# Optimization experiments

Hardware: AMD Instinct MI355X
Metric: run time of the kernel (lower is better)

Reference implementation:

```python
import jax, jax.numpy as jnp
import numpy as np

BATCH = 8
TABLE_NUM = 16          # levels L
TABLE_DIM = 8192        # entries per table
RES_MIN, RES_MAX = 16, 256
SAMPLE_RES = 256
N = SAMPLE_RES * SAMPLE_RES
CH = TABLE_NUM * 2      # feature dim per level is 2
STYLE_DIM = 512
PRIME = np.uint32(2654435761)
LN_EPS = 1e-5
DEMOD_EPS = 1e-8

# geometric level resolutions (Instant-NGP style)
_b = np.exp((np.log(RES_MAX) - np.log(RES_MIN)) / (TABLE_NUM - 1))
RES_LIST = [int(np.floor(RES_MIN * (_b ** l))) for l in range(TABLE_NUM)]


def _corner_idx_weights(coords):
    """coords [N,2] in [0,1] -> (idx [L,N,4] int32 flat into L*T, w [L,N,4])."""
    idx_all, w_all = [], []
    for l, res in enumerate(RES_LIST):
        pos = coords * (res - 1)                     # [N,2]
        p0f = jnp.floor(pos)
        frac = pos - p0f                              # bilinear fractions
        p0 = jnp.clip(p0f.astype(jnp.int32), 0, res - 2)
        x0, y0 = p0[:, 0], p0[:, 1]
        x1, y1 = x0 + 1, y0 + 1
        fx, fy = frac[:, 0], frac[:, 1]
        cx = jnp.stack([x0, x1, x0, x1], -1)          # [N,4]
        cy = jnp.stack([y0, y0, y1, y1], -1)
        w = jnp.stack([(1 - fx) * (1 - fy), fx * (1 - fy),
                       (1 - fx) * fy, fx * fy], -1)   # [N,4]
        if res * res <= TABLE_DIM:                    # dense grid fits: direct index
            idx = cy * res + cx
        else:                                         # spatial hash
            h = cx.astype(jnp.uint32) ^ (cy.astype(jnp.uint32) * PRIME)
            idx = (h % jnp.uint32(TABLE_DIM)).astype(jnp.int32)
        idx_all.append(idx + l * TABLE_DIM)
        w_all.append(w)
    return jnp.stack(idx_all), jnp.stack(w_all)       # [L,N,4]


def _hash_retrieve(tables, idx, w):
    """tables [B,L,T,2] -> bilinear multi-res lookup [B,N,2L]."""
    B = tables.shape[0]
    tf = tables.reshape(B, TABLE_NUM * TABLE_DIM, 2)
    g = tf[:, idx.reshape(-1)]                        # [B, L*N*4, 2]
    g = g.reshape(B, TABLE_NUM, N, 4, 2)
    feats = jnp.einsum('blncf,lnc->blnf', g, w)       # [B,L,N,2]
    return feats.transpose(0, 2, 1, 3).reshape(B, N, CH)


def _hash_recon(tokens, idx, w):
    """tokens [B,N,2L] -> transpose scatter back into tables [B,L,T,2]."""
    B = tokens.shape[0]
    t = tokens.reshape(B, N, TABLE_NUM, 2).transpose(0, 2, 1, 3)   # [B,L,N,2]
    contrib = jnp.einsum('blnf,lnc->blncf', t, w)                   # [B,L,N,4,2]
    out = jnp.zeros((B, TABLE_NUM * TABLE_DIM, 2), tokens.dtype)
    out = out.at[:, idx.reshape(-1)].add(contrib.reshape(B, -1, 2))
    return out.reshape(B, TABLE_NUM, TABLE_DIM, 2)


def _synthesis_layer(x, s, affine_w, affine_b, conv_w, conv_b):
    """StyleGAN2 modulated 3x3 conv (demodulate, up=1) + bias + lrelu*sqrt(2)."""
    styles = s @ (affine_w.T / np.sqrt(STYLE_DIM)) + affine_b       # [B,ch]
    xm = x * styles[:, :, None, None]                               # modulate input
    y = jax.lax.conv_general_dilated(xm, conv_w, (1, 1), [(1, 1), (1, 1)],
                                     dimension_numbers=('NCHW', 'OIHW', 'NCHW'))
    # demod coef: rsqrt(sum_{i,k,l} (w_oikl * style_i)^2 + eps)
    dcoef = jax.lax.rsqrt(jnp.einsum('oikl,bi->bo', conv_w * conv_w,
                                     styles * styles) + DEMOD_EPS)
    y = y * dcoef[:, :, None, None] + conv_b[None, :, None, None]
    return jax.nn.leaky_relu(y, 0.2) * np.sqrt(2.0)


def setup_inputs() -> dict:
    key = jax.random.key(0)
    k1, k2, k3, k4 = jax.random.split(key, 4)
    inputs = jax.random.normal(k1, (BATCH, TABLE_NUM, 2 * TABLE_DIM), jnp.float32)
    s = jax.random.normal(k2, (BATCH, STYLE_DIM), jnp.float32)
    g = jnp.linspace(0.0, 1.0, SAMPLE_RES)
    yy, xx = jnp.meshgrid(g, g, indexing='ij')
    coords = jnp.stack([xx, yy], -1).reshape(N, 2).astype(jnp.float32)
    affine_w = jax.random.normal(k3, (CH, STYLE_DIM), jnp.float32)
    affine_b = jnp.ones((CH,), jnp.float32)          # bias_init=1
    conv_w = jax.random.normal(k4, (CH, CH, 3, 3), jnp.float32)
    conv_b = jnp.zeros((CH,), jnp.float32)
    return {"inputs": inputs, "s": s, "coords": coords,
            "affine_w": affine_w, "affine_b": affine_b,
            "conv_w": conv_w, "conv_b": conv_b}


def reference(inputs, s, coords, affine_w, affine_b, conv_w, conv_b):
    B = inputs.shape[0]
    tables = inputs.reshape(B, TABLE_NUM, TABLE_DIM, 2)
    idx, w = _corner_idx_weights(coords)
    feats = _hash_retrieve(tables, idx, w)                 # [B,N,ch]
    block = feats.reshape(B, SAMPLE_RES, SAMPLE_RES, CH).transpose(0, 3, 1, 2)
    block = _synthesis_layer(block, s, affine_w, affine_b, conv_w, conv_b)
    tokens = block.reshape(B, CH, N).transpose(0, 2, 1)    # [B,N,ch]
    recon = _hash_recon(tokens, idx, w)                    # [B,L,T,2]
    out = recon.reshape(B, TABLE_NUM, -1) + inputs         # residual
    mu = out.mean(-1, keepdims=True)
    var = ((out - mu) ** 2).mean(-1, keepdims=True)
    return (out - mu) * jax.lax.rsqrt(var + LN_EPS)        # layer_norm, no affine
```

## Files before the change

### kernel.cpp

```cpp
#include <hip/hip_runtime.h>
#include <cmath>
#include <cstdint>

#define NB 8
#define NL 16
#define TD 8192
#define NPIX 65536
#define CH 32
#define SD 512

static constexpr uint32_t PRIME = 2654435761u;

typedef __attribute__((ext_vector_type(8))) short bf16x8;
typedef __attribute__((ext_vector_type(4))) float f32x4;

static constexpr int cNCX[16] = {4,5,5,5,6,6,7,7,8,9,10,12,13,15,18,20};
static constexpr int CTOFF[17] = {0,16,41,66,91,127,163,212,261,325,406,506,650,819,1044,1368,1768};

struct LevelParams {
    int res[NL];
    int hashed[NL];
    int uoff[NL];
    int soff[NL];
    int cwoff[NL];
    int nck[NL];
    int sumr;
    int nwaves;
};

__device__ __forceinline__ unsigned short f2bf(float f) {
    uint32_t u = __float_as_uint(f);
    return (unsigned short)((u + 0x7fffu + ((u >> 16) & 1u)) >> 16);
}
__device__ __forceinline__ float bflo(uint32_t u) { return __uint_as_float(u << 16); }
__device__ __forceinline__ float bfhi(uint32_t u) { return __uint_as_float(u & 0xffff0000u); }
__device__ __forceinline__ uint32_t packbf(float a, float b) {
    return (uint32_t)f2bf(a) | ((uint32_t)f2bf(b) << 16);
}

__global__ __launch_bounds__(256) void k_prep(
    const float* __restrict__ s, const float* __restrict__ aw,
    const float* __restrict__ ab, const float* __restrict__ cw,
    const float* __restrict__ coords,
    float* __restrict__ styles, float* __restrict__ dcoef,
    int* __restrict__ ctab, float* __restrict__ ftab, int* __restrict__ stab,
    unsigned short* __restrict__ wpack, LevelParams p) {
    int bb = blockIdx.x;
    int t = threadIdx.x;
    if (bb < NB) {
        int b = bb;
        int c = t >> 3, part = t & 7;
        const float* sv = s + b * SD + part * 64;
        const float* wv = aw + c * SD + part * 64;
        float acc = 0.f;
        #pragma unroll 8
        for (int k = 0; k < 64; ++k) acc += sv[k] * wv[k];
        acc += __shfl_xor(acc, 1, 64);
        acc += __shfl_xor(acc, 2, 64);
        acc += __shfl_xor(acc, 4, 64);
        __shared__ float st_sh[CH];
        if (part == 0) {
            float st = acc * 0.04419417382415922f  + ab[c];
            styles[b * CH + c] = st;
            st_sh[c] = st;
        }
        __syncthreads();
        if (t < CH) {
            float d = 0.f;
            for (int i = 0; i < CH; ++i) {
                const float* w9 = cw + (t * CH + i) * 9;
                float ws = 0.f;
                #pragma unroll
                for (int k = 0; k < 9; ++k) ws += w9[k] * w9[k];
                float si = st_sh[i];
                d += ws * si * si;
            }
            dcoef[b * CH + t] = rsqrtf(d + 1e-8f);
        }
    } else if (bb < NB + NL) {
        int l = bb - NB;
        int j = t;
        int r = p.res[l];
        float g = coords[2 * j];
        float px = g * (float)(r - 1);
        float fl = floorf(px);
        float f = px - fl;
        int c = min((int)fl, r - 2);
        ctab[l * 256 + j] = c;
        ftab[l * 256 + j] = f;
        __shared__ int cs[256];
        cs[j] = c;
        __syncthreads();
        for (int cc = j; cc <= r; cc += 256) {
            int cnt = 0;
            for (int i = 0; i < 256; ++i) cnt += (cs[i] < cc) ? 1 : 0;
            stab[p.soff[l] + cc] = cnt;
        }
    } else {
        int idx = (bb - NB - NL) * 256 + t;
        if (idx < 9 * 4 * 32 * 8) {
            int j = idx & 7;
            int o = (idx >> 3) & 31;
            int kgi = (idx >> 8) & 3;
            int tap = idx >> 10;
            wpack[idx] = f2bf(cw[(o * 32 + kgi * 8 + j) * 9 + tap]);
        }
    }
}

struct P1S { float fx[4], fy[4]; uint32_t cor[4][4]; };

template<int L0>
__device__ __forceinline__ void p1_loadcvrv(int pl, const float2* col2, const float2* row2,
                                            float2 cv[4], float2 rv[4]) {
    int rr = pl / 18, cc = pl - rr * 18;
    cv[0] = col2[(L0 + 0) * 18 + cc]; rv[0] = row2[(L0 + 0) * 18 + rr];
    cv[1] = col2[(L0 + 1) * 18 + cc]; rv[1] = row2[(L0 + 1) * 18 + rr];
    cv[2] = col2[(L0 + 2) * 18 + cc]; rv[2] = row2[(L0 + 2) * 18 + rr];
    cv[3] = col2[(L0 + 3) * 18 + cc]; rv[3] = row2[(L0 + 3) * 18 + rr];
}

template<int L0>
__device__ __forceinline__ void p1_issue(const float2 cv[4], const float2 rv[4],
                                         const uint32_t* ctile, P1S& st) {
    #pragma unroll
    for (int k = 0; k < 4; ++k) {
        int a = CTOFF[L0 + k] + __float_as_int(rv[k].x) * cNCX[L0 + k] + __float_as_int(cv[k].x);
        st.cor[k][0] = ctile[a];
        st.cor[k][1] = ctile[a + 1];
        st.cor[k][2] = ctile[a + cNCX[L0 + k]];
        st.cor[k][3] = ctile[a + cNCX[L0 + k] + 1];
        st.fx[k] = cv[k].y;
        st.fy[k] = rv[k].y;
    }
}

template<int L0>
__device__ __forceinline__ void p1_emit(int pl, int tx0, int ty0,
                                        const P1S& st, uint32_t* xt) {
    constexpr int q = L0 / 4;
    int rr = pl / 18, cc = pl - rr * 18;
    int gy = ty0 + rr - 1, gx = tx0 + cc - 1;
    uint4 v = make_uint4(0u, 0u, 0u, 0u);
    if (pl < 324 && (unsigned)gy < 256u && (unsigned)gx < 256u) {
        #pragma unroll
        for (int k = 0; k < 4; ++k) {
            float fx = st.fx[k], fy = st.fy[k];
            float w00 = (1.f - fx) * (1.f - fy), w10 = fx * (1.f - fy);
            float w01 = (1.f - fx) * fy,         w11 = fx * fy;
            float f0 = w00 * bflo(st.cor[k][0]) + w10 * bflo(st.cor[k][1])
                     + w01 * bflo(st.cor[k][2]) + w11 * bflo(st.cor[k][3]);
            float f1 = w00 * bfhi(st.cor[k][0]) + w10 * bfhi(st.cor[k][1])
                     + w01 * bfhi(st.cor[k][2]) + w11 * bfhi(st.cor[k][3]);
            (&v.x)[k] = packbf(f0, f1);
        }
    }
    if (pl < 324)
        *(uint4*)(xt + (size_t)(pl * 4 + (q ^ (cc & 3))) * 4) = v;
}

template<int L0>
__device__ __forceinline__ void phase1(int lane, int tx0, int ty0,
                                       const float2* col2, const float2* row2,
                                       const uint32_t* ctile, uint32_t* xt) {
    float2 cvN[4], rvN[4];
    P1S sA, sB;
    p1_loadcvrv<L0>(lane, col2, row2, cvN, rvN);
    p1_issue<L0>(cvN, rvN, ctile, sA);
    p1_loadcvrv<L0>(min(64 + lane, 323), col2, row2, cvN, rvN);
    #pragma unroll
    for (int it2 = 0; it2 < 3; ++it2) {
        {
            int it = 2 * it2;
            p1_issue<L0>(cvN, rvN, ctile, sB);
            p1_loadcvrv<L0>(min((it + 2) * 64 + lane, 323), col2, row2, cvN, rvN);
            p1_emit<L0>(it * 64 + lane, tx0, ty0, sA, xt);
        }
        {
            int it = 2 * it2 + 1;
            p1_issue<L0>(cvN, rvN, ctile, sA);
            p1_loadcvrv<L0>(min((it + 2) * 64 + lane, 323), col2, row2, cvN, rvN);
            p1_emit<L0>(it * 64 + lane, tx0, ty0, sB, xt);
        }
    }
}

__global__ __launch_bounds__(256) void k_conv(
    const float* __restrict__ tables, const int* __restrict__ ctab,
    const float* __restrict__ ftab, const float* __restrict__ styles,
    const unsigned short* __restrict__ wpack, const float* __restrict__ cb,
    const float* __restrict__ dcoef, uint32_t* __restrict__ tokens,
    LevelParams p) {
    __shared__ uint32_t xt[18 * 18 * 16];
    __shared__ uint32_t ctile[1768];
    __shared__ float2 col2[NL * 18];
    __shared__ float2 row2[NL * 18];
    __shared__ int cxbase[NL], cybase[NL], ncxA[NL], ncyA[NL];

    int bid = blockIdx.x;
    int b = bid & 7;
    int t = bid >> 3;
    int tx0 = (t & 15) * 16, ty0 = (t >> 4) * 16;
    int tid = threadIdx.x;
    int lane = tid & 63, wv = tid >> 6;
    int npx = lane & 15, kg = lane >> 4;
    const float* tb = tables + (size_t)b * NL * TD * 2;

    if (tid < NL) {
        int l = tid;
        int cxb = ctab[l * 256 + max(tx0 - 1, 0)];
        int cyb = ctab[l * 256 + max(ty0 - 1, 0)];
        cxbase[l] = cxb;
        cybase[l] = cyb;
        ncxA[l] = ctab[l * 256 + min(tx0 + 16, 255)] - cxb + 2;
        ncyA[l] = ctab[l * 256 + min(ty0 + 16, 255)] - cyb + 2;
    }
    __syncthreads();

    for (int u0 = tid; u0 < NL * 36; u0 += 256) {
        int l = u0 / 36, pos = u0 - l * 36;
        if (pos < 18) {
            int gx = tx0 - 1 + pos;
            int gxc = min(max(gx, 0), 255);
            col2[l * 18 + pos] = make_float2(
                __int_as_float(ctab[l * 256 + gxc] - cxbase[l]), ftab[l * 256 + gxc]);
        } else {
            int pr = pos - 18;
            int gy = ty0 - 1 + pr;
            int gyc = min(max(gy, 0), 255);
            row2[l * 18 + pr] = make_float2(
                __int_as_float(ctab[l * 256 + gyc] - cybase[l]), ftab[l * 256 + gyc]);
        }
    }

    #pragma unroll
    for (int l = 0; l < NL; ++l) {
        const int NCXl = cNCX[l];
        const int CAP = (CTOFF[l + 1] - CTOFF[l]);
        float s0 = styles[b * CH + 2 * l], s1 = styles[b * CH + 2 * l + 1];
        for (int u2 = tid; u2 < CAP; u2 += 256) {
            int sy = u2 / NCXl;
            int sx = u2 - sy * NCXl;
            if (sx < ncxA[l] && sy < ncyA[l]) {
                int ax = cxbase[l] + sx, ay = cybase[l] + sy;
                int r = p.res[l];
                uint32_t idx = p.hashed[l]
                    ? (((uint32_t)ax ^ ((uint32_t)ay * PRIME)) & (TD - 1))
                    : (uint32_t)(ay * r + ax);
                float2 g = *(const float2*)(tb + (size_t)l * TD * 2 + 2 * idx);
                ctile[CTOFF[l] + sy * NCXl + sx] = packbf(g.x * s0, g.y * s1);
            }
        }
    }
    __syncthreads();

    switch (wv) {
        case 0: phase1<0>(lane, tx0, ty0, col2, row2, ctile, xt); break;
        case 1: phase1<4>(lane, tx0, ty0, col2, row2, ctile, xt); break;
        case 2: phase1<8>(lane, tx0, ty0, col2, row2, ctile, xt); break;
        default: phase1<12>(lane, tx0, ty0, col2, row2, ctile, xt); break;
    }
    __builtin_amdgcn_sched_barrier(0);

    bf16x8 wf[9][2];
    #pragma unroll
    for (int tp = 0; tp < 9; ++tp) {
        wf[tp][0] = *(const bf16x8*)(wpack + (size_t)((tp * 4 + kg) * 32 + npx) * 8);
        wf[tp][1] = *(const bf16x8*)(wpack + (size_t)((tp * 4 + kg) * 32 + 16 + npx) * 8);
    }
    float dc[2][4], bs[2][4];
    #pragma unroll
    for (int ob = 0; ob < 2; ++ob)
        #pragma unroll
        for (int rg = 0; rg < 4; ++rg) {
            int oc = ob * 16 + kg * 4 + rg;
            dc[ob][rg] = dcoef[b * CH + oc];
            bs[ob][rg] = cb[oc];
        }
    __syncthreads();

    #pragma unroll 1
    for (int it = 0; it < 4; ++it) {
        int py_l = it * 4 + wv;
        int px_l = npx;
        f32x4 a0 = {0.f, 0.f, 0.f, 0.f};
        f32x4 a1 = {0.f, 0.f, 0.f, 0.f};
        #pragma unroll
        for (int ky = 0; ky < 3; ++ky) {
            int rowb = (py_l + ky) * 18;
            #pragma unroll
            for (int kx = 0; kx < 3; ++kx) {
                int cc = px_l + kx;
                bf16x8 bf = *(const bf16x8*)(xt + (((rowb + cc) << 2) + (kg ^ (cc & 3))) * 4);
                a0 = __builtin_amdgcn_mfma_f32_16x16x32_bf16(wf[ky * 3 + kx][0], bf, a0, 0, 0, 0);
                a1 = __builtin_amdgcn_mfma_f32_16x16x32_bf16(wf[ky * 3 + kx][1], bf, a1, 0, 0, 0);
            }
        }
        int py = ty0 + py_l, px = tx0 + px_l;
        size_t pbase = (size_t)py * 256 + px;
        {
            float y0 = a0[0] * dc[0][0] + bs[0][0];
            float y1 = a0[1] * dc[0][1] + bs[0][1];
            float y2 = a0[2] * dc[0][2] + bs[0][2];
            float y3 = a0[3] * dc[0][3] + bs[0][3];
            y0 = (y0 > 0.f ? y0 : 0.2f * y0) * 1.4142135623730951f;
            y1 = (y1 > 0.f ? y1 : 0.2f * y1) * 1.4142135623730951f;
            y2 = (y2 > 0.f ? y2 : 0.2f * y2) * 1.4142135623730951f;
            y3 = (y3 > 0.f ? y3 : 0.2f * y3) * 1.4142135623730951f;
            int lp0 = kg * 2;
            tokens[((size_t)(b * NL + lp0)) * NPIX + pbase] = packbf(y0, y1);
            tokens[((size_t)(b * NL + lp0 + 1)) * NPIX + pbase] = packbf(y2, y3);
        }
        {
            float y0 = a1[0] * dc[1][0] + bs[1][0];
            float y1 = a1[1] * dc[1][1] + bs[1][1];
            float y2 = a1[2] * dc[1][2] + bs[1][2];
            float y3 = a1[3] * dc[1][3] + bs[1][3];
            y0 = (y0 > 0.f ? y0 : 0.2f * y0) * 1.4142135623730951f;
            y1 = (y1 > 0.f ? y1 : 0.2f * y1) * 1.4142135623730951f;
            y2 = (y2 > 0.f ? y2 : 0.2f * y2) * 1.4142135623730951f;
            y3 = (y3 > 0.f ? y3 : 0.2f * y3) * 1.4142135623730951f;
            int lp0 = 8 + kg * 2;
            tokens[((size_t)(b * NL + lp0)) * NPIX + pbase] = packbf(y0, y1);
            tokens[((size_t)(b * NL + lp0 + 1)) * NPIX + pbase] = packbf(y2, y3);
        }
    }
}

__global__ __launch_bounds__(256) void k_recon1(const uint32_t* __restrict__ tokens,
                                                const int* __restrict__ ctab,
                                                const float* __restrict__ ftab,
                                                const int* __restrict__ stab,
                                                float* __restrict__ U, LevelParams p) {
    __shared__ float2 cf[256];
    __shared__ int sl[260];
    __shared__ uint32_t tok[4][256];
    int l = blockIdx.x >> 6;
    int grp = blockIdx.x & 63;
    int b = blockIdx.y;
    int tid = threadIdx.x;
    int lane = tid & 63, wv = tid >> 6;
    int r = p.res[l];

    cf[tid] = make_float2(__int_as_float(ctab[l * 256 + tid]), ftab[l * 256 + tid]);
    for (int q = tid; q <= r; q += 256) sl[q] = stab[p.soff[l] + q];
    int i = grp * 4 + wv;
    const uint32_t* trow = tokens + (size_t)(b * NL + l) * NPIX + i * 256;
    *(uint4*)&tok[wv][lane * 4] = *(const uint4*)(trow + lane * 4);
    __syncthreads();

    float* Ul = U + (size_t)b * (p.sumr * 512) + p.uoff[l] + (size_t)i * r * 2;
    int nck = p.nck[l];
    #pragma unroll 1
    for (int ck = 0; ck < nck; ++ck) {
        int cx = ck * 64 + lane;
        bool valid = cx < r;
        int jlo = 0, jhi = -1;
        if (valid) {
            jlo = (cx > 0) ? sl[cx - 1] : 0;
            jhi = sl[min(cx + 1, r)] - 1;
        }
        float a0 = 0.f, a1 = 0.f;
        for (int j = jlo; j <= jhi; ++j) {
            float2 cfv = cf[j];
            int c = __float_as_int(cfv.x);
            float f = cfv.y;
            float w = (c == cx) ? (1.f - f) : f;
            uint32_t tv = tok[wv][j];
            a0 += w * bflo(tv);
            a1 += w * bfhi(tv);
        }
        if (valid)
            *(float2*)(Ul + cx * 2) = make_float2(a0, a1);
    }
}

__global__ __launch_bounds__(256) void k_recon2(const float* __restrict__ U,
                                                const int* __restrict__ ctab,
                                                const float* __restrict__ ftab,
                                                const int* __restrict__ stab,
                                                float* __restrict__ R, LevelParams p) {
    int wid = blockIdx.x * 4 + (threadIdx.x >> 6);
    int lane = threadIdx.x & 63;
    int b = blockIdx.y;
    if (wid >= p.nwaves) return;
    int l = 0;
    #pragma unroll
    for (int q = 1; q < NL; ++q) if (wid >= p.cwoff[q]) l = q;
    int u = wid - p.cwoff[l];
    int r = p.res[l];
    int nck = p.nck[l];
    int cy = u / nck;
    int ck = u - cy * nck;
    int cx = ck * 64 + lane;
    bool valid = cx < r;
    const int* Sl = stab + p.soff[l];
    int ilo = (cy > 0) ? Sl[cy - 1] : 0;
    int ihi = Sl[min(cy + 1, r)] - 1;
    const float* Ub = U + (size_t)b * (p.sumr * 512) + p.uoff[l];
    const int* crow = ctab + l * 256;
    const float* frow = ftab + l * 256;
    float a0 = 0.f, a1 = 0.f;
    for (int i = ilo; i <= ihi; ++i) {
        int c = crow[i];
        float f = frow[i];
        float w = (c == cy) ? (1.f - f) : f;
        if (valid) {
            float2 uu = *(const float2*)(Ub + ((size_t)i * r + cx) * 2);
            a0 += w * uu.x;
            a1 += w * uu.y;
        }
    }
    if (!valid) return;
    float* Rbl = R + (size_t)(b * NL + l) * TD * 2;
    if (p.hashed[l]) {
        uint32_t h = ((uint32_t)cx ^ ((uint32_t)cy * PRIME)) & (TD - 1);
        atomicAdd(&Rbl[2 * h], a0);
        atomicAdd(&Rbl[2 * h + 1], a1);
    } else {
        *(float2*)(Rbl + 2 * (cy * r + cx)) = make_float2(a0, a1);
    }
}

__global__ __launch_bounds__(512) void k_ln(const float* __restrict__ R,
                                            const float* __restrict__ inp,
                                            float* __restrict__ out) {
    int row = blockIdx.x;
    const float4* rv = (const float4*)(R + (size_t)row * 16384);
    const float4* iv = (const float4*)(inp + (size_t)row * 16384);
    int tid = threadIdx.x;
    float sum = 0.f, ssq = 0.f;
    for (int k = tid; k < 4096; k += 512) {
        float4 a = rv[k], c = iv[k];
        float x0 = a.x + c.x, x1 = a.y + c.y, x2 = a.z + c.z, x3 = a.w + c.w;
        sum += x0 + x1 + x2 + x3;
        ssq += x0 * x0 + x1 * x1 + x2 * x2 + x3 * x3;
    }
    #pragma unroll
    for (int off = 32; off > 0; off >>= 1) {
        sum += __shfl_xor(sum, off, 64);
        ssq += __shfl_xor(ssq, off, 64);
    }
    __shared__ float red[16];
    int w = tid >> 6;
    if ((tid & 63) == 0) { red[w * 2] = sum; red[w * 2 + 1] = ssq; }
    __syncthreads();
    sum = 0.f; ssq = 0.f;
    #pragma unroll
    for (int q = 0; q < 8; ++q) { sum += red[q * 2]; ssq += red[q * 2 + 1]; }
    float mu = sum * (1.f / 16384.f);
    float var = ssq * (1.f / 16384.f) - mu * mu;
    float inv = rsqrtf(var + 1e-5f);
    float4* ob = (float4*)(out + (size_t)row * 16384);
    for (int k = tid; k < 4096; k += 512) {
        float4 a = rv[k], c = iv[k];
        float4 o4;
        o4.x = (a.x + c.x - mu) * inv;
        o4.y = (a.y + c.y - mu) * inv;
        o4.z = (a.z + c.z - mu) * inv;
        o4.w = (a.w + c.w - mu) * inv;
        ob[k] = o4;
    }
}

extern "C" void kernel_launch(void* const* d_in, const int* in_sizes, int n_in,
                              void* d_out, int out_size, void* d_ws, size_t ws_size,
                              hipStream_t stream) {
    const float* inputs = (const float*)d_in[0];
    const float* s      = (const float*)d_in[1];
    const float* coords = (const float*)d_in[2];
    const float* aw     = (const float*)d_in[3];
    const float* ab     = (const float*)d_in[4];
    const float* cw     = (const float*)d_in[5];
    const float* cb     = (const float*)d_in[6];

    char* ws = (char*)d_ws;
    float*    U      = (float*)(ws);
    uint32_t* tokens = (uint32_t*)(ws + 33554432);
    float*    R      = (float*)(ws + 67108864);
    float*    styles = (float*)(ws + 75497472);
    float*    dcoef  = (float*)(ws + 75498496);
    int*      ctab   = (int*)(ws + 75499520);
    float*    ftab   = (float*)(ws + 75515904);
    int*      stab   = (int*)(ws + 75532288);
    unsigned short* wpack = (unsigned short*)(ws + 75540480);

    LevelParams p;
    double bb = exp((log(256.0) - log(16.0)) / 15.0);
    int uoff = 0, soff = 0, cwoff = 0;
    for (int l = 0; l < NL; ++l) {
        int r = (int)floor(16.0 * pow(bb, (double)l));
        p.res[l] = r;
        p.hashed[l] = (r * r > TD) ? 1 : 0;
        p.uoff[l] = uoff;
        p.soff[l] = soff;
        p.cwoff[l] = cwoff;
        int nck = (r + 63) >> 6;
        p.nck[l] = nck;
        uoff += r * 512;
        soff += r + 2;
        cwoff += r * nck;
    }
    p.sumr = uoff / 512;
    p.nwaves = cwoff;

    hipMemsetAsync(R, 0, (size_t)NB * NL * TD * 2 * sizeof(float), stream);
    hipLaunchKernelGGL(k_prep, dim3(NB + NL + 36), dim3(256), 0, stream,
                       s, aw, ab, cw, coords, styles, dcoef, ctab, ftab, stab, wpack, p);
    hipLaunchKernelGGL(k_conv, dim3(2048), dim3(256), 0, stream,
                       inputs, ctab, ftab, styles, wpack, cb, dcoef, tokens, p);
    hipLaunchKernelGGL(k_recon1, dim3(NL * 64, NB), dim3(256), 0, stream,
                       tokens, ctab, ftab, stab, U, p);
    hipLaunchKernelGGL(k_recon2, dim3((p.nwaves + 3) / 4, NB), dim3(256), 0, stream,
                       U, ctab, ftab, stab, R, p);
    hipLaunchKernelGGL(k_ln, dim3(NB * NL), dim3(512), 0, stream,
                       R, inputs, (float*)d_out);
}
```

Before: 114.0 us.

## Split bilinear tile interpolation into separable x then y passes with aliased LDS

Bilinear interpolation of the hash-grid corner tile now runs as two separable passes. An x-pass writes horizontally interpolated values per corner row and output column into a new LDS buffer. A y-pass then blends two of those rows per pixel and level. This removes redundant corner loads and weight products across pixels that share rows, and LDS regions are aliased into one array so the extra buffer fits. The cost is an additional __syncthreads, the per-position level search, and a dropped software pipeline, since the y-pass loop is no longer unrolled.

```diff
diff --git a/kernel.cpp b/kernel.cpp
--- a/kernel.cpp
+++ b/kernel.cpp
@@ -16,6 +16,7 @@
 
 static constexpr int cNCX[16] = {4,5,5,5,6,6,7,7,8,9,10,12,13,15,18,20};
 static constexpr int CTOFF[17] = {0,16,41,66,91,127,163,212,261,325,406,506,650,819,1044,1368,1768};
+static constexpr int PAOFF[17] = {0,72,162,252,342,450,558,684,810,954,1116,1296,1512,1746,2016,2340,2700};
 
 struct LevelParams {
     int res[NL];
@@ -108,80 +109,33 @@
     }
 }
 
-struct P1S { float fx[4], fy[4]; uint32_t cor[4][4]; };
-
 template<int L0>
-__device__ __forceinline__ void p1_loadcvrv(int pl, const float2* col2, const float2* row2,
-                                            float2 cv[4], float2 rv[4]) {
-    int rr = pl / 18, cc = pl - rr * 18;
-    cv[0] = col2[(L0 + 0) * 18 + cc]; rv[0] = row2[(L0 + 0) * 18 + rr];
-    cv[1] = col2[(L0 + 1) * 18 + cc]; rv[1] = row2[(L0 + 1) * 18 + rr];
-    cv[2] = col2[(L0 + 2) * 18 + cc]; rv[2] = row2[(L0 + 2) * 18 + rr];
-    cv[3] = col2[(L0 + 3) * 18 + cc]; rv[3] = row2[(L0 + 3) * 18 + rr];
-}
-
-template<int L0>
-__device__ __forceinline__ void p1_issue(const float2 cv[4], const float2 rv[4],
-                                         const uint32_t* ctile, P1S& st) {
-    #pragma unroll
-    for (int k = 0; k < 4; ++k) {
-        int a = CTOFF[L0 + k] + __float_as_int(rv[k].x) * cNCX[L0 + k] + __float_as_int(cv[k].x);
-        st.cor[k][0] = ctile[a];
-        st.cor[k][1] = ctile[a + 1];
-        st.cor[k][2] = ctile[a + cNCX[L0 + k]];
-        st.cor[k][3] = ctile[a + cNCX[L0 + k] + 1];
-        st.fx[k] = cv[k].y;
-        st.fy[k] = rv[k].y;
-    }
-}
-
-template<int L0>
-__device__ __forceinline__ void p1_emit(int pl, int tx0, int ty0,
-                                        const P1S& st, uint32_t* xt) {
+__device__ __forceinline__ void passB(int lane, int tx0, int ty0,
+                                      const float2* xtmp, const float2* row2,
+                                      uint32_t* xt) {
     constexpr int q = L0 / 4;
-    int rr = pl / 18, cc = pl - rr * 18;
-    int gy = ty0 + rr - 1, gx = tx0 + cc - 1;
-    uint4 v = make_uint4(0u, 0u, 0u, 0u);
-    if (pl < 324 && (unsigned)gy < 256u && (unsigned)gx < 256u) {
-        #pragma unroll
-        for (int k = 0; k < 4; ++k) {
-            float fx = st.fx[k], fy = st.fy[k];
-            float w00 = (1.f - fx) * (1.f - fy), w10 = fx * (1.f - fy);
-            float w01 = (1.f - fx) * fy,         w11 = fx * fy;
-            float f0 = w00 * bflo(st.cor[k][0]) + w10 * bflo(st.cor[k][1])
-                     + w01 * bflo(st.cor[k][2]) + w11 * bflo(st.cor[k][3]);
-            float f1 = w00 * bfhi(st.cor[k][0]) + w10 * bfhi(st.cor[k][1])
-                     + w01 * bfhi(st.cor[k][2]) + w11 * bfhi(st.cor[k][3]);
-            (&v.x)[k] = packbf(f0, f1);
-        }
-    }
-    if (pl < 324)
-        *(uint4*)(xt + (size_t)(pl * 4 + (q ^ (cc & 3))) * 4) = v;
-}
-
-template<int L0>
-__device__ __forceinline__ void phase1(int lane, int tx0, int ty0,
-                                       const float2* col2, const float2* row2,
-                                       const uint32_t* ctile, uint32_t* xt) {
-    float2 cvN[4], rvN[4];
-    P1S sA, sB;
-    p1_loadcvrv<L0>(lane, col2, row2, cvN, rvN);
-    p1_issue<L0>(cvN, rvN, ctile, sA);
-    p1_loadcvrv<L0>(min(64 + lane, 323), col2, row2, cvN, rvN);
-    #pragma unroll
-    for (int it2 = 0; it2 < 3; ++it2) {
-        {
-            int it = 2 * it2;
-            p1_issue<L0>(cvN, rvN, ctile, sB);
-            p1_loadcvrv<L0>(min((it + 2) * 64 + lane, 323), col2, row2, cvN, rvN);
-            p1_emit<L0>(it * 64 + lane, tx0, ty0, sA, xt);
-        }
-        {
-            int it = 2 * it2 + 1;
-            p1_issue<L0>(cvN, rvN, ctile, sA);
-            p1_loadcvrv<L0>(min((it + 2) * 64 + lane, 323), col2, row2, cvN, rvN);
-            p1_emit<L0>(it * 64 + lane, tx0, ty0, sB, xt);
-        }
+    #pragma unroll 1
+    for (int it = 0; it < 6; ++it) {
+        int pl = it * 64 + lane;
+        int rr = pl / 18, cc = pl - rr * 18;
+        int gy = ty0 + rr - 1, gx = tx0 + cc - 1;
+        uint4 v = make_uint4(0u, 0u, 0u, 0u);
+        bool in = (pl < 324) && ((unsigned)gy < 256u) && ((unsigned)gx < 256u);
+        if (in) {
+            #pragma unroll
+            for (int k = 0; k < 4; ++k) {
+                float2 rv = row2[(L0 + k) * 18 + rr];
+                int base = PAOFF[L0 + k] + __float_as_int(rv.x) * 18 + cc;
+                float fy = rv.y;
+                float2 lo = xtmp[base];
+                float2 hi = xtmp[base + 18];
+                float f0 = (1.f - fy) * lo.x + fy * hi.x;
+                float f1 = (1.f - fy) * lo.y + fy * hi.y;
+                (&v.x)[k] = packbf(f0, f1);
+            }
+        }
+        if (pl < 324)
+            *(uint4*)(xt + (size_t)(pl * 4 + (q ^ (cc & 3))) * 4) = v;
     }
 }
 
@@ -191,11 +145,13 @@
     const unsigned short* __restrict__ wpack, const float* __restrict__ cb,
     const float* __restrict__ dcoef, uint32_t* __restrict__ tokens,
     LevelParams p) {
-    __shared__ uint32_t xt[18 * 18 * 16];
-    __shared__ uint32_t ctile[1768];
-    __shared__ float2 col2[NL * 18];
-    __shared__ float2 row2[NL * 18];
+    __shared__ uint32_t smem[11160];
     __shared__ int cxbase[NL], cybase[NL], ncxA[NL], ncyA[NL];
+    uint32_t* ctile = smem;
+    float2*  col2  = (float2*)(smem + 1768);
+    uint32_t* xt   = smem;
+    float2*  xtmp  = (float2*)(smem + 5184);
+    float2*  row2  = (float2*)(smem + 5184 + 5400);
 
     int bid = blockIdx.x;
     int b = bid & 7;
@@ -254,11 +210,27 @@
     }
     __syncthreads();
 
+    for (int pos = tid; pos < 2700; pos += 256) {
+        int l = 0;
+        #pragma unroll
+        for (int q = 1; q < NL; ++q) if (pos >= PAOFF[q]) l = q;
+        int rem = pos - PAOFF[l];
+        int sy = rem / 18, px = rem - sy * 18;
+        float2 cv = col2[l * 18 + px];
+        int a = CTOFF[l] + sy * cNCX[l] + __float_as_int(cv.x);
+        float fx = cv.y;
+        uint32_t c0 = ctile[a], c1 = ctile[a + 1];
+        float t0 = (1.f - fx) * bflo(c0) + fx * bflo(c1);
+        float t1 = (1.f - fx) * bfhi(c0) + fx * bfhi(c1);
+        xtmp[pos] = make_float2(t0, t1);
+    }
+    __syncthreads();
+
     switch (wv) {
-        case 0: phase1<0>(lane, tx0, ty0, col2, row2, ctile, xt); break;
-        case 1: phase1<4>(lane, tx0, ty0, col2, row2, ctile, xt); break;
-        case 2: phase1<8>(lane, tx0, ty0, col2, row2, ctile, xt); break;
-        default: phase1<12>(lane, tx0, ty0, col2, row2, ctile, xt); break;
+        case 0: passB<0>(lane, tx0, ty0, xtmp, row2, xt); break;
+        case 1: passB<4>(lane, tx0, ty0, xtmp, row2, xt); break;
+        case 2: passB<8>(lane, tx0, ty0, xtmp, row2, xt); break;
+        default: passB<12>(lane, tx0, ty0, xtmp, row2, xt); break;
     }
     __builtin_amdgcn_sched_barrier(0);
 
```

Result: slower. 128.6 us (+12.8%).
